# Performance work log

Hardware: AMD Instinct MI355X
Metric: run time of the kernel (lower is better)

Reference implementation:

```python
import jax, jax.numpy as jnp
import numpy as np

EPS = 1e-12  # matches torch F.normalize default eps


def _l2_normalize(x):
    # F.normalize: x / max(||x||_2, eps), along last dim
    n = jnp.sqrt(jnp.sum(x * x, axis=-1, keepdims=True))
    return x / jnp.maximum(n, EPS)


def setup_inputs() -> dict:
    key = jax.random.key(0)
    k1, k2, k3, k4 = jax.random.split(key, 4)
    N, M, D = 2048, 100000, 256
    return {
        "shape_embedding": jax.random.normal(k1, (N, D), dtype=jnp.float32),
        "gallery_embedding": jax.random.normal(k2, (M, D), dtype=jnp.float32),
        "category_idx": jax.random.randint(k3, (M,), 0, 9, dtype=jnp.int64) if jax.config.jax_enable_x64 else jax.random.randint(k3, (M,), 0, 9, dtype=jnp.int32),
        "shape_idx": jax.random.randint(k4, (M,), 0, 10000, dtype=jnp.int32),
    }


def reference(shape_embedding, gallery_embedding, category_idx, shape_idx):
    # Gallery embeddings are L2-normalized once in __init__; query normalized per call.
    g = _l2_normalize(gallery_embedding)          # [M, D]
    q = _l2_normalize(shape_embedding)            # [N, D]
    scores = jnp.einsum('nd,md->nm', q, g)        # cosine similarity [N, M]
    idx = jnp.argmax(scores, axis=-1)             # top-1 retrieval [N]
    return category_idx[idx], shape_idx[idx]
```

## Files before the change

kernel.cpp:

```cpp
#include <hip/hip_runtime.h>
#include <hip/hip_fp16.h>
#include <math.h>
#include <float.h>

#define M_G 100000
#define M_PAD 100032
#define NT64 1563
#define N_Q 2048
#define DIM 256
#define NG 3126
#define GSTR 3136
#define MARGIN 0.009f

typedef _Float16 f16x8 __attribute__((ext_vector_type(8)));
typedef float f32x4 __attribute__((ext_vector_type(4)));

#define WS_GP 0
#define WS_QP 51216384
#define WS_BM 52264960

__device__ inline unsigned pack_h2(float a, float b) {
    __half ha = __float2half(a), hb = __float2half(b);
    return (unsigned)*(unsigned short*)&ha | ((unsigned)*(unsigned short*)&hb << 16);
}
__device__ inline void gload_lds16(const void* gsrc, void* ldst) {
    __builtin_amdgcn_global_load_lds(
        (const __attribute__((address_space(1))) unsigned int*)gsrc,
        (__attribute__((address_space(3))) unsigned int*)ldst, 16, 0, 0);
}

#define BAR __builtin_amdgcn_s_barrier()
#define LGKM0 { asm volatile("s_waitcnt lgkmcnt(0)" ::: "memory"); \
                __builtin_amdgcn_sched_barrier(0); }
#define VMCNT(n) { asm volatile("s_waitcnt vmcnt(" #n ")" ::: "memory"); \
                   __builtin_amdgcn_sched_barrier(0); }

__global__ __launch_bounds__(256) void pack_kernel(
    const float* __restrict__ g, const float* __restrict__ q,
    uint4* __restrict__ gp, uint4* __restrict__ qp)
{
    const int b = blockIdx.x;
    const int w4 = threadIdx.x >> 6, lane = threadIdx.x & 63;
    const bool isg = b < (M_PAD / 4);
    const int row = (isg ? b : b - M_PAD / 4) * 4 + w4;
    const bool real = !isg || row < M_G;
    const float* src = isg ? g + (size_t)row * DIM : q + (size_t)row * DIM;

    float inv = 0.0f;
    if (real) {
        float4 v = ((const float4*)src)[lane];
        float ss = v.x * v.x + v.y * v.y + v.z * v.z + v.w * v.w;
        #pragma unroll
        for (int o = 32; o; o >>= 1) ss += __shfl_xor(ss, o);
        inv = 1.0f / fmaxf(sqrtf(ss), 1e-12f);
    }
    if (lane < 32) {
        uint4 w = make_uint4(0u, 0u, 0u, 0u);
        if (real) {
            float4 a = ((const float4*)src)[lane * 2];
            float4 c = ((const float4*)src)[lane * 2 + 1];
            w.x = pack_h2(a.x * inv, a.y * inv);
            w.y = pack_h2(a.z * inv, a.w * inv);
            w.z = pack_h2(c.x * inv, c.y * inv);
            w.w = pack_h2(c.z * inv, c.w * inv);
        }
        const int kt = lane >> 3, gg = lane & 7;
        if (isg) {
            int mt = row >> 6, rl = row & 63;
            gp[((size_t)mt * 4 + kt) * 512 + rl * 8 + (gg ^ (rl & 7))] = w;
        } else {
            int qt = row >> 8, rl = row & 255;
            qp[((size_t)qt * 4 + kt) * 2048 + rl * 8 + (gg ^ (rl & 7))] = w;
        }
    }
}

#define STAGE32(dstbase, src) { const uint4* s_ = (src); _Pragma("unroll") \
  for (int p_ = 0; p_ < 4; ++p_) \
    gload_lds16(s_ + p_ * 512 + tid, lds + (dstbase) + (p_ * 512 + tid) * 16); }

#define READ_BP(KT, bufbase) { _Pragma("unroll") \
  for (int nj = 0; nj < 4; ++nj) { \
    const char* p_ = lds + (bufbase) + (wc * 64 + nj * 16 + r16) * 128; \
    bR[KT][0][nj] = *(const f16x8*)(p_ + sw0); \
    bR[KT][1][nj] = *(const f16x8*)(p_ + sw1); } }

#define PREF(d0, d1, KT, SW) { \
    d0 = *(const f16x8*)(pb + (KT) * 8192 + (SW)); \
    d1 = *(const f16x8*)(pb + (KT) * 8192 + 2048 + (SW)); }

#define MFMA8(A0, A1, KT, KK) { _Pragma("unroll") \
  for (int nj = 0; nj < 4; ++nj) { \
    acc[0][nj] = __builtin_amdgcn_mfma_f32_16x16x32_f16( \
        A0, bR[KT][KK][nj], acc[0][nj], 0, 0, 0); \
    acc[1][nj] = __builtin_amdgcn_mfma_f32_16x16x32_f16( \
        A1, bR[KT][KK][nj], acc[1][nj], 0, 0, 0); } }

__global__ __launch_bounds__(512, 2) void scoreA_kernel(
    const uint4* __restrict__ gp, const uint4* __restrict__ qp,
    unsigned short* __restrict__ bmaxH)
{
    extern __shared__ char lds[];

    const int bid = blockIdx.x;
    const int qt = bid >> 6, mc = bid & 63;
    const int nt = (mc < 27) ? 25 : 24;
    const int t0 = (mc < 27) ? mc * 25 : 675 + (mc - 27) * 24;

    const int tid = threadIdx.x;
    const int wid = tid >> 6, lane = tid & 63;
    const int wr = wid >> 2, wc = wid & 3;
    const int r16 = lane & 15, rhi = lane >> 4;
    const int sw0 = ((rhi ^ (r16 & 7)) << 4);
    const int sw1 = (((4 + rhi) ^ (r16 & 7)) << 4);

    const uint4* qsrc = qp + (size_t)qt * 8192;

    f16x8 bR[4][2][4];
    STAGE32(0,     qsrc + 0 * 2048);
    STAGE32(32768, qsrc + 1 * 2048);
    VMCNT(4); BAR;
    READ_BP(0, 0); BAR;
    STAGE32(0, qsrc + 2 * 2048);
    VMCNT(4); BAR;
    READ_BP(1, 32768); BAR;
    STAGE32(32768, qsrc + 3 * 2048);
    VMCNT(4); BAR;
    READ_BP(2, 0); BAR;
    STAGE32(0, gp + (size_t)t0 * 2048);
    VMCNT(4); BAR;
    READ_BP(3, 32768); BAR;
    VMCNT(0); BAR;

    for (int t = 0; t < nt; ++t) {
        const int mtile = t0 + t;
        const int cur = (t & 1) << 15;
        const int nxt = cur ^ 32768;
        if (t + 1 < nt) STAGE32(nxt, gp + (size_t)(mtile + 1) * 2048);

        f32x4 acc[2][4];
        #pragma unroll
        for (int mi = 0; mi < 2; ++mi)
            #pragma unroll
            for (int nj = 0; nj < 4; ++nj) acc[mi][nj] = (f32x4){0.f, 0.f, 0.f, 0.f};

        const char* pb = lds + cur + (wr * 32 + r16) * 128;
        f16x8 aA0, aA1, aB0, aB1;
        PREF(aA0, aA1, 0, sw0);
        PREF(aB0, aB1, 0, sw1);  MFMA8(aA0, aA1, 0, 0);
        PREF(aA0, aA1, 1, sw0);  MFMA8(aB0, aB1, 0, 1);
        PREF(aB0, aB1, 1, sw1);  MFMA8(aA0, aA1, 1, 0);
        PREF(aA0, aA1, 2, sw0);  MFMA8(aB0, aB1, 1, 1);
        PREF(aB0, aB1, 2, sw1);  MFMA8(aA0, aA1, 2, 0);
        PREF(aA0, aA1, 3, sw0);  MFMA8(aB0, aB1, 2, 1);
        PREF(aB0, aB1, 3, sw1);  MFMA8(aA0, aA1, 3, 0);
        MFMA8(aB0, aB1, 3, 1);

        float cm[4] = {-FLT_MAX, -FLT_MAX, -FLT_MAX, -FLT_MAX};
        #pragma unroll
        for (int mi = 0; mi < 2; ++mi)
            #pragma unroll
            for (int jj = 0; jj < 4; ++jj)
                #pragma unroll
                for (int nj = 0; nj < 4; ++nj)
                    cm[nj] = fmaxf(cm[nj], acc[mi][nj][jj]);
        const bool padgrp = (mtile * 64 + wr * 32) >= M_G;
        #pragma unroll
        for (int nj = 0; nj < 4; ++nj) {
            float v = cm[nj];
            v = fmaxf(v, __shfl_xor(v, 16));
            v = fmaxf(v, __shfl_xor(v, 32));
            if (lane < 16) {
                int qn = qt * 256 + wc * 64 + nj * 16 + lane;
                __half h = __float2half(padgrp ? -65504.f : v);
                bmaxH[(size_t)qn * GSTR + mtile * 2 + wr] = *(unsigned short*)&h;
            }
        }
        if (t + 1 < nt) { VMCNT(8); BAR; }
    }
}

__global__ __launch_bounds__(256) void phaseB_kernel(
    const float* __restrict__ q, const float* __restrict__ g,
    const unsigned short* __restrict__ bmaxH,
    const int* __restrict__ cat, const int* __restrict__ shp,
    int* __restrict__ out)
{
    __shared__ __align__(16) float qrow[DIM];
    __shared__ int glist[NG];
    __shared__ int ng;
    __shared__ float smax[4];
    __shared__ float rbs[4];
    __shared__ int rbi[4];

    const int qi = blockIdx.x;
    const int tid = threadIdx.x;
    const int lane = tid & 63, wid = tid >> 6;
    const __half* bm = (const __half*)(bmaxH + (size_t)qi * GSTR);
    if (tid < 64)
        *(float4*)&qrow[tid * 4] = *(const float4*)(q + (size_t)qi * DIM + tid * 4);
    if (tid == 0) ng = 0;

    float m = -FLT_MAX;
    for (int gr = tid; gr < NG; gr += 256)
        m = fmaxf(m, __half2float(bm[gr]));
    #pragma unroll
    for (int o = 32; o; o >>= 1) m = fmaxf(m, __shfl_xor(m, o));
    if (lane == 0) smax[wid] = m;
    __syncthreads();
    const float thr = fmaxf(fmaxf(smax[0], smax[1]), fmaxf(smax[2], smax[3])) - MARGIN;

    for (int gr = tid; gr < NG; gr += 256)
        if (__half2float(bm[gr]) >= thr)
            glist[atomicAdd(&ng, 1)] = gr;
    __syncthreads();

    float bs = -FLT_MAX;
    int bi = 0x7fffffff;
    const int r = tid >> 3, p = tid & 7;
    const int n = ng;
    for (int i = 0; i < n; ++i) {
        int mm = glist[i] * 32 + r;
        if (mm < M_G) {
            const float* grow = g + (size_t)mm * DIM + p * 32;
            const float* qr = qrow + p * 32;
            float s = 0.f, ssq = 0.f;
            #pragma unroll
            for (int jj = 0; jj < 8; ++jj) {
                float4 gv = *(const float4*)(grow + jj * 4);
                float4 qv = *(const float4*)(qr + jj * 4);
                s += gv.x * qv.x + gv.y * qv.y + gv.z * qv.z + gv.w * qv.w;
                ssq += gv.x * gv.x + gv.y * gv.y + gv.z * gv.z + gv.w * gv.w;
            }
            s += __shfl_xor(s, 1);  s += __shfl_xor(s, 2);  s += __shfl_xor(s, 4);
            ssq += __shfl_xor(ssq, 1); ssq += __shfl_xor(ssq, 2); ssq += __shfl_xor(ssq, 4);
            s *= 1.0f / fmaxf(sqrtf(ssq), 1e-12f);
            if (p == 0 && (s > bs || (s == bs && mm < bi))) { bs = s; bi = mm; }
        }
    }
    #pragma unroll
    for (int o = 1; o < 64; o <<= 1) {
        float os = __shfl_xor(bs, o);
        int oi = __shfl_xor(bi, o);
        if (os > bs || (os == bs && oi < bi)) { bs = os; bi = oi; }
    }
    if (lane == 0) { rbs[wid] = bs; rbi[wid] = bi; }
    __syncthreads();
    if (tid == 0) {
        #pragma unroll
        for (int ww = 1; ww < 4; ++ww)
            if (rbs[ww] > bs || (rbs[ww] == bs && rbi[ww] < bi)) { bs = rbs[ww]; bi = rbi[ww]; }
        out[qi] = cat[bi];
        out[N_Q + qi] = shp[bi];
    }
}

extern "C" void kernel_launch(void* const* d_in, const int* in_sizes, int n_in,
                              void* d_out, int out_size, void* d_ws, size_t ws_size,
                              hipStream_t stream) {
    const float* q = (const float*)d_in[0];
    const float* g = (const float*)d_in[1];
    const int* cat = (const int*)d_in[2];
    const int* shp = (const int*)d_in[3];
    int* out = (int*)d_out;

    char* ws = (char*)d_ws;
    uint4* gp             = (uint4*)(ws + WS_GP);
    uint4* qp             = (uint4*)(ws + WS_QP);
    unsigned short* bmaxH = (unsigned short*)(ws + WS_BM);

    hipFuncSetAttribute((const void*)scoreA_kernel,
                        hipFuncAttributeMaxDynamicSharedMemorySize, 65536);

    pack_kernel<<<M_PAD / 4 + N_Q / 4, 256, 0, stream>>>(g, q, gp, qp);
    scoreA_kernel<<<512, 512, 65536, stream>>>(gp, qp, bmaxH);
    phaseB_kernel<<<N_Q, 256, 0, stream>>>(q, g, bmaxH, cat, shp, out);
}
```

Measured before the change: 166.7 us.

## Switch score kernel to 32x32x16 MFMA with split accumulators and XCD-aware block mapping

Replaces the 16x16x32 MFMA tiling with 32x32x16 MFMA instructions. The B operand is reorganized into 16 k-slices and the A fragment reads are interleaved with two independent accumulator chains, shortening the dependent MFMA chain. Block indices are remapped so that consecutive blocks on the same XCD share gallery tiles across query tiles, which should improve L2 reuse. The row-max epilogue now needs fewer shuffles, and the vmcnt wait is tightened; both carry some risk of LDS bank conflicts or wrong wait counts.

```diff
diff --git a/kernel.cpp b/kernel.cpp
--- a/kernel.cpp
+++ b/kernel.cpp
@@ -13,7 +13,7 @@
 #define MARGIN 0.009f
 
 typedef _Float16 f16x8 __attribute__((ext_vector_type(8)));
-typedef float f32x4 __attribute__((ext_vector_type(4)));
+typedef float f32x16 __attribute__((ext_vector_type(16)));
 
 #define WS_GP 0
 #define WS_QP 51216384
@@ -79,22 +79,21 @@
   for (int p_ = 0; p_ < 4; ++p_) \
     gload_lds16(s_ + p_ * 512 + tid, lds + (dstbase) + (p_ * 512 + tid) * 16); }
 
-#define READ_BP(KT, bufbase) { _Pragma("unroll") \
-  for (int nj = 0; nj < 4; ++nj) { \
-    const char* p_ = lds + (bufbase) + (wc * 64 + nj * 16 + r16) * 128; \
-    bR[KT][0][nj] = *(const f16x8*)(p_ + sw0); \
-    bR[KT][1][nj] = *(const f16x8*)(p_ + sw1); } }
-
-#define PREF(d0, d1, KT, SW) { \
-    d0 = *(const f16x8*)(pb + (KT) * 8192 + (SW)); \
-    d1 = *(const f16x8*)(pb + (KT) * 8192 + 2048 + (SW)); }
-
-#define MFMA8(A0, A1, KT, KK) { _Pragma("unroll") \
-  for (int nj = 0; nj < 4; ++nj) { \
-    acc[0][nj] = __builtin_amdgcn_mfma_f32_16x16x32_f16( \
-        A0, bR[KT][KK][nj], acc[0][nj], 0, 0, 0); \
-    acc[1][nj] = __builtin_amdgcn_mfma_f32_16x16x32_f16( \
-        A1, bR[KT][KK][nj], acc[1][nj], 0, 0, 0); } }
+#define READ_BQ(KT, bufbase) { _Pragma("unroll") \
+  for (int sl_ = 0; sl_ < 4; ++sl_) { _Pragma("unroll") \
+    for (int cb_ = 0; cb_ < 2; ++cb_) \
+      bR[(KT) * 4 + sl_][cb_] = *(const f16x8*)(lds + (bufbase) + qroff + \
+          cb_ * 4096 + ((((sl_ << 1) + lh) ^ l7) << 4)); } }
+
+#define RD_A(S) (*(const f16x8*)(pb + ((S) >> 2) * 8192 + \
+    ((((((S) & 3) << 1) + lh) ^ l7) << 4)))
+
+#define MFMA32(AV, S) { \
+    acc[0] = __builtin_amdgcn_mfma_f32_32x32x16_f16(AV, bR[S][0], acc[0], 0, 0, 0); \
+    acc[1] = __builtin_amdgcn_mfma_f32_32x32x16_f16(AV, bR[S][1], acc[1], 0, 0, 0); }
+#define MFMB32(AV, S) { \
+    accb[0] = __builtin_amdgcn_mfma_f32_32x32x16_f16(AV, bR[S][0], accb[0], 0, 0, 0); \
+    accb[1] = __builtin_amdgcn_mfma_f32_32x32x16_f16(AV, bR[S][1], accb[1], 0, 0, 0); }
 
 __global__ __launch_bounds__(512, 2) void scoreA_kernel(
     const uint4* __restrict__ gp, const uint4* __restrict__ qp,
@@ -103,33 +102,35 @@
     extern __shared__ char lds[];
 
     const int bid = blockIdx.x;
-    const int qt = bid >> 6, mc = bid & 63;
+    const int xcd = bid & 7;
+    const int qt = (bid >> 3) & 7;
+    const int mc = (bid >> 6) * 8 + xcd;
     const int nt = (mc < 27) ? 25 : 24;
     const int t0 = (mc < 27) ? mc * 25 : 675 + (mc - 27) * 24;
 
     const int tid = threadIdx.x;
     const int wid = tid >> 6, lane = tid & 63;
     const int wr = wid >> 2, wc = wid & 3;
-    const int r16 = lane & 15, rhi = lane >> 4;
-    const int sw0 = ((rhi ^ (r16 & 7)) << 4);
-    const int sw1 = (((4 + rhi) ^ (r16 & 7)) << 4);
+    const int l31 = lane & 31, lh = lane >> 5, l7 = lane & 7;
+    const int qroff = (wc * 64 + l31) * 128;
+    const int aroff = (wr * 32 + l31) * 128;
 
     const uint4* qsrc = qp + (size_t)qt * 8192;
 
-    f16x8 bR[4][2][4];
+    f16x8 bR[16][2];
     STAGE32(0,     qsrc + 0 * 2048);
     STAGE32(32768, qsrc + 1 * 2048);
     VMCNT(4); BAR;
-    READ_BP(0, 0); BAR;
+    READ_BQ(0, 0); LGKM0; BAR;
     STAGE32(0, qsrc + 2 * 2048);
     VMCNT(4); BAR;
-    READ_BP(1, 32768); BAR;
+    READ_BQ(1, 32768); LGKM0; BAR;
     STAGE32(32768, qsrc + 3 * 2048);
     VMCNT(4); BAR;
-    READ_BP(2, 0); BAR;
+    READ_BQ(2, 0); LGKM0; BAR;
     STAGE32(0, gp + (size_t)t0 * 2048);
     VMCNT(4); BAR;
-    READ_BP(3, 32768); BAR;
+    READ_BQ(3, 32768); LGKM0; BAR;
     VMCNT(0); BAR;
 
     for (int t = 0; t < nt; ++t) {
@@ -138,45 +139,41 @@
         const int nxt = cur ^ 32768;
         if (t + 1 < nt) STAGE32(nxt, gp + (size_t)(mtile + 1) * 2048);
 
-        f32x4 acc[2][4];
-        #pragma unroll
-        for (int mi = 0; mi < 2; ++mi)
+        f32x16 acc[2], accb[2];
+        #pragma unroll
+        for (int c = 0; c < 2; ++c)
             #pragma unroll
-            for (int nj = 0; nj < 4; ++nj) acc[mi][nj] = (f32x4){0.f, 0.f, 0.f, 0.f};
-
-        const char* pb = lds + cur + (wr * 32 + r16) * 128;
-        f16x8 aA0, aA1, aB0, aB1;
-        PREF(aA0, aA1, 0, sw0);
-        PREF(aB0, aB1, 0, sw1);  MFMA8(aA0, aA1, 0, 0);
-        PREF(aA0, aA1, 1, sw0);  MFMA8(aB0, aB1, 0, 1);
-        PREF(aB0, aB1, 1, sw1);  MFMA8(aA0, aA1, 1, 0);
-        PREF(aA0, aA1, 2, sw0);  MFMA8(aB0, aB1, 1, 1);
-        PREF(aB0, aB1, 2, sw1);  MFMA8(aA0, aA1, 2, 0);
-        PREF(aA0, aA1, 3, sw0);  MFMA8(aB0, aB1, 2, 1);
-        PREF(aB0, aB1, 3, sw1);  MFMA8(aA0, aA1, 3, 0);
-        MFMA8(aB0, aB1, 3, 1);
-
-        float cm[4] = {-FLT_MAX, -FLT_MAX, -FLT_MAX, -FLT_MAX};
-        #pragma unroll
-        for (int mi = 0; mi < 2; ++mi)
-            #pragma unroll
-            for (int jj = 0; jj < 4; ++jj)
-                #pragma unroll
-                for (int nj = 0; nj < 4; ++nj)
-                    cm[nj] = fmaxf(cm[nj], acc[mi][nj][jj]);
+            for (int i = 0; i < 16; ++i) { acc[c][i] = 0.f; accb[c][i] = 0.f; }
+
+        const char* pb = lds + cur + aroff;
+        f16x8 aP, aQ;
+        aP = RD_A(0);
+        #pragma unroll
+        for (int sp = 0; sp < 8; ++sp) {
+            aQ = RD_A(2 * sp + 1);
+            MFMA32(aP, 2 * sp);
+            if (sp < 7) aP = RD_A(2 * sp + 2);
+            MFMB32(aQ, 2 * sp + 1);
+        }
+
+        const int group = mtile * 2 + wr;
         const bool padgrp = (mtile * 64 + wr * 32) >= M_G;
         #pragma unroll
-        for (int nj = 0; nj < 4; ++nj) {
-            float v = cm[nj];
-            v = fmaxf(v, __shfl_xor(v, 16));
+        for (int cb = 0; cb < 2; ++cb) {
+            f32x16 f = acc[cb] + accb[cb];
+            float m0 = fmaxf(fmaxf(fmaxf(f[0], f[1]), fmaxf(f[2], f[3])),
+                             fmaxf(fmaxf(f[4], f[5]), fmaxf(f[6], f[7])));
+            float m1 = fmaxf(fmaxf(fmaxf(f[8], f[9]), fmaxf(f[10], f[11])),
+                             fmaxf(fmaxf(f[12], f[13]), fmaxf(f[14], f[15])));
+            float v = fmaxf(m0, m1);
             v = fmaxf(v, __shfl_xor(v, 32));
-            if (lane < 16) {
-                int qn = qt * 256 + wc * 64 + nj * 16 + lane;
+            if (lane < 32) {
+                int qn = qt * 256 + wc * 64 + cb * 32 + l31;
                 __half h = __float2half(padgrp ? -65504.f : v);
-                bmaxH[(size_t)qn * GSTR + mtile * 2 + wr] = *(unsigned short*)&h;
+                bmaxH[(size_t)qn * GSTR + group] = *(unsigned short*)&h;
             }
         }
-        if (t + 1 < nt) { VMCNT(8); BAR; }
+        if (t + 1 < nt) { VMCNT(2); BAR; }
     }
 }
 
```

Measured after the change: 170.6 us. 2.3% more time.

## Give each wave a private LDS gallery buffer and remap blocks by XCD

Applied to the files above, without the earlier changes.

The score kernel's shared double-buffered gallery tile becomes a 16KB LDS region per wave. Each wave loads its own gallery rows and prefetches the next tile per k-slice right after reading the current one, so the block-wide barriers in the main loop go away. Block indices are also remapped so that blocks on the same XCD share gallery chunks. The costs are a dynamic LDS allocation of 128KB, which likely allows only one block per CU, and gallery rows duplicated across the four column-waves, which raises L2-to-LDS traffic.

```diff
diff --git a/kernel.cpp b/kernel.cpp
--- a/kernel.cpp
+++ b/kernel.cpp
@@ -79,15 +79,18 @@
   for (int p_ = 0; p_ < 4; ++p_) \
     gload_lds16(s_ + p_ * 512 + tid, lds + (dstbase) + (p_ * 512 + tid) * 16); }
 
+#define STAGE_Q(ts, KT) { const uint4* s_ = (ts) + (KT) * 512 + wr * 256; \
+  _Pragma("unroll") for (int p_ = 0; p_ < 4; ++p_) \
+    gload_lds16(s_ + p_ * 64 + lane, myr + (KT) * 4096 + (p_ * 64 + lane) * 16); }
+
 #define READ_BP(KT, bufbase) { _Pragma("unroll") \
   for (int nj = 0; nj < 4; ++nj) { \
     const char* p_ = lds + (bufbase) + (wc * 64 + nj * 16 + r16) * 128; \
     bR[KT][0][nj] = *(const f16x8*)(p_ + sw0); \
     bR[KT][1][nj] = *(const f16x8*)(p_ + sw1); } }
 
-#define PREF(d0, d1, KT, SW) { \
-    d0 = *(const f16x8*)(pb + (KT) * 8192 + (SW)); \
-    d1 = *(const f16x8*)(pb + (KT) * 8192 + 2048 + (SW)); }
+#define RD_AQ(KT, KK, F) \
+    (*(const f16x8*)(myr + (KT) * 4096 + ((F) * 16 + r16) * 128 + ((KK) ? sw1 : sw0)))
 
 #define MFMA8(A0, A1, KT, KK) { _Pragma("unroll") \
   for (int nj = 0; nj < 4; ++nj) { \
@@ -103,7 +106,9 @@
     extern __shared__ char lds[];
 
     const int bid = blockIdx.x;
-    const int qt = bid >> 6, mc = bid & 63;
+    const int xcd = bid & 7;
+    const int qt = (bid >> 3) & 7;
+    const int mc = (bid >> 6) * 8 + xcd;
     const int nt = (mc < 27) ? 25 : 24;
     const int t0 = (mc < 27) ? mc * 25 : 675 + (mc - 27) * 24;
 
@@ -113,6 +118,7 @@
     const int r16 = lane & 15, rhi = lane >> 4;
     const int sw0 = ((rhi ^ (r16 & 7)) << 4);
     const int sw1 = (((4 + rhi) ^ (r16 & 7)) << 4);
+    char* myr = lds + wid * 16384;
 
     const uint4* qsrc = qp + (size_t)qt * 8192;
 
@@ -120,23 +126,26 @@
     STAGE32(0,     qsrc + 0 * 2048);
     STAGE32(32768, qsrc + 1 * 2048);
     VMCNT(4); BAR;
-    READ_BP(0, 0); BAR;
+    READ_BP(0, 0); LGKM0; BAR;
     STAGE32(0, qsrc + 2 * 2048);
     VMCNT(4); BAR;
-    READ_BP(1, 32768); BAR;
+    READ_BP(1, 32768); LGKM0; BAR;
     STAGE32(32768, qsrc + 3 * 2048);
     VMCNT(4); BAR;
-    READ_BP(2, 0); BAR;
-    STAGE32(0, gp + (size_t)t0 * 2048);
-    VMCNT(4); BAR;
-    READ_BP(3, 32768); BAR;
+    READ_BP(2, 0); LGKM0; BAR;
     VMCNT(0); BAR;
+    READ_BP(3, 32768); LGKM0; BAR;
+
+    {
+        const uint4* ts = gp + (size_t)t0 * 2048;
+        STAGE_Q(ts, 0); STAGE_Q(ts, 1); STAGE_Q(ts, 2); STAGE_Q(ts, 3);
+    }
+    VMCNT(0);
 
     for (int t = 0; t < nt; ++t) {
         const int mtile = t0 + t;
-        const int cur = (t & 1) << 15;
-        const int nxt = cur ^ 32768;
-        if (t + 1 < nt) STAGE32(nxt, gp + (size_t)(mtile + 1) * 2048);
+        const bool pf = (t + 1 < nt);
+        const uint4* nsrc = gp + (size_t)(mtile + 1) * 2048;
 
         f32x4 acc[2][4];
         #pragma unroll
@@ -144,17 +153,15 @@
             #pragma unroll
             for (int nj = 0; nj < 4; ++nj) acc[mi][nj] = (f32x4){0.f, 0.f, 0.f, 0.f};
 
-        const char* pb = lds + cur + (wr * 32 + r16) * 128;
-        f16x8 aA0, aA1, aB0, aB1;
-        PREF(aA0, aA1, 0, sw0);
-        PREF(aB0, aB1, 0, sw1);  MFMA8(aA0, aA1, 0, 0);
-        PREF(aA0, aA1, 1, sw0);  MFMA8(aB0, aB1, 0, 1);
-        PREF(aB0, aB1, 1, sw1);  MFMA8(aA0, aA1, 1, 0);
-        PREF(aA0, aA1, 2, sw0);  MFMA8(aB0, aB1, 1, 1);
-        PREF(aB0, aB1, 2, sw1);  MFMA8(aA0, aA1, 2, 0);
-        PREF(aA0, aA1, 3, sw0);  MFMA8(aB0, aB1, 2, 1);
-        PREF(aB0, aB1, 3, sw1);  MFMA8(aA0, aA1, 3, 0);
-        MFMA8(aB0, aB1, 3, 1);
+        #pragma unroll
+        for (int kt = 0; kt < 4; ++kt) {
+            f16x8 a00 = RD_AQ(kt, 0, 0), a01 = RD_AQ(kt, 0, 1);
+            f16x8 a10 = RD_AQ(kt, 1, 0), a11 = RD_AQ(kt, 1, 1);
+            LGKM0;
+            if (pf) STAGE_Q(nsrc, kt);
+            MFMA8(a00, a01, kt, 0);
+            MFMA8(a10, a11, kt, 1);
+        }
 
         float cm[4] = {-FLT_MAX, -FLT_MAX, -FLT_MAX, -FLT_MAX};
         #pragma unroll
@@ -164,6 +171,7 @@
                 #pragma unroll
                 for (int nj = 0; nj < 4; ++nj)
                     cm[nj] = fmaxf(cm[nj], acc[mi][nj][jj]);
+        const int group = mtile * 2 + wr;
         const bool padgrp = (mtile * 64 + wr * 32) >= M_G;
         #pragma unroll
         for (int nj = 0; nj < 4; ++nj) {
@@ -173,10 +181,10 @@
             if (lane < 16) {
                 int qn = qt * 256 + wc * 64 + nj * 16 + lane;
                 __half h = __float2half(padgrp ? -65504.f : v);
-                bmaxH[(size_t)qn * GSTR + mtile * 2 + wr] = *(unsigned short*)&h;
+                bmaxH[(size_t)qn * GSTR + group] = *(unsigned short*)&h;
             }
         }
-        if (t + 1 < nt) { VMCNT(8); BAR; }
+        if (pf) { VMCNT(4); }
     }
 }
 
@@ -270,9 +278,9 @@
     unsigned short* bmaxH = (unsigned short*)(ws + WS_BM);
 
     hipFuncSetAttribute((const void*)scoreA_kernel,
-                        hipFuncAttributeMaxDynamicSharedMemorySize, 65536);
+                        hipFuncAttributeMaxDynamicSharedMemorySize, 131072);
 
     pack_kernel<<<M_PAD / 4 + N_Q / 4, 256, 0, stream>>>(g, q, gp, qp);
-    scoreA_kernel<<<512, 512, 65536, stream>>>(gp, qp, bmaxH);
+    scoreA_kernel<<<512, 512, 131072, stream>>>(gp, qp, bmaxH);
     phaseB_kernel<<<N_Q, 256, 0, stream>>>(q, g, bmaxH, cat, shp, out);
 }
```

Measured after the change: 174.7 us. 1.05x slower.
